# Kernel tuning notes

Measured on AMD Instinct MI355X. Metric: run time of the kernel, lower is better.

## Reference

```python
import jax, jax.numpy as jnp
import numpy as np

B, N, D, H, P = 4, 512, 256, 8, 3
HD = D // H
EPS = 1e-5

def _ln(x, g, b):
    m = jnp.mean(x, axis=-1, keepdims=True)
    v = jnp.var(x, axis=-1, keepdims=True)
    return (x - m) * jax.lax.rsqrt(v + EPS) * g + b

def setup_inputs() -> dict:
    key = jax.random.key(0)
    ks = jax.random.split(key, 12)
    s = lambda *sh: 1.0 / np.sqrt(sh[0])
    return {
        "x": jax.random.normal(ks[0], (B, N, D), jnp.float32),
        "mask": jax.random.randint(ks[1], (B, N), 0, 2).astype(bool),
        "pair_feat": jax.random.normal(ks[2], (B, N, N, P), jnp.float32),
        "Wqkv": jax.random.normal(ks[3], (D, 3 * D), jnp.float32) * s(D),
        "Wout": jax.random.normal(ks[4], (D, D), jnp.float32) * s(D),
        "bout": jnp.zeros((D,), jnp.float32),
        "Wp1": jax.random.normal(ks[5], (P, D), jnp.float32) * s(P),
        "bp1": jnp.zeros((D,), jnp.float32),
        "Wp2": jax.random.normal(ks[6], (D, H), jnp.float32) * s(D),
        "bp2": jnp.zeros((H,), jnp.float32),
        "Wf1": jax.random.normal(ks[7], (D, 4 * D), jnp.float32) * s(D),
        "bf1": jnp.zeros((4 * D,), jnp.float32),
        "Wf2": jax.random.normal(ks[8], (4 * D, D), jnp.float32) * s(4 * D),
        "bf2": jnp.zeros((D,), jnp.float32),
        "g1": jnp.ones((D,), jnp.float32), "b1": jnp.zeros((D,), jnp.float32),
        "g2": jnp.ones((D,), jnp.float32), "b2": jnp.zeros((D,), jnp.float32),
    }

def reference(x, mask, pair_feat, Wqkv, Wout, bout, Wp1, bp1, Wp2, bp2,
              Wf1, bf1, Wf2, bf2, g1, b1, g2, b2):
    b_, n_, d_ = x.shape
    scale = HD ** -0.5
    qkv = x @ Wqkv                                  # [B,N,3D]
    q, k, v = jnp.split(qkv, 3, axis=-1)
    q = q.reshape(b_, n_, H, HD)
    k = k.reshape(b_, n_, H, HD)
    v = v.reshape(b_, n_, H, HD)
    logits = jnp.einsum('bihd,bjhd->bhij', q, k) * scale
    # pairwise bias MLP -> per-head bias [B,H,N,N]
    bias = jax.nn.relu(pair_feat @ Wp1 + bp1) @ Wp2 + bp2   # [B,N,N,H]
    logits = logits + jnp.transpose(bias, (0, 3, 1, 2))
    key_mask = ~mask[:, None, None, :]               # [B,1,1,N]
    logits = jnp.where(key_mask, -1e9, logits)
    attn = jax.nn.softmax(logits, axis=-1)
    out = jnp.einsum('bhij,bjhd->bihd', attn, v).reshape(b_, n_, d_)
    out = out @ Wout + bout
    x = _ln(x + out, g1, b1)
    h = jax.nn.gelu(x @ Wf1 + bf1, approximate=False) @ Wf2 + bf2
    return _ln(x + h, g2, b2)
```

## Files before the change

### kernel.cpp

```cpp
#include <hip/hip_runtime.h>
#include <hip/hip_fp16.h>
#include <math.h>

typedef unsigned short u16;
typedef short s16x8 __attribute__((ext_vector_type(8)));
typedef _Float16 f16x8 __attribute__((ext_vector_type(8)));
typedef float f32x4 __attribute__((ext_vector_type(4)));
typedef unsigned int u32x2 __attribute__((ext_vector_type(2)));

constexpr int CB = 4, CN = 512, CD = 256, CH = 8, CHD = 32;
constexpr float CEPS = 1e-5f;
constexpr int M_ROWS = CB * CN;
constexpr float QSCALE = 0.17677669529663687f;

constexpr size_t O_XB    = 0;
constexpr size_t O_QB    = 1048576;
constexpr size_t O_KB    = 2097152;
constexpr size_t O_VT    = 3145728;
constexpr size_t O_WQKVT = 4194304;
constexpr size_t O_WOUTT = O_WQKVT + 393216;
constexpr size_t O_WF1T  = O_WOUTT + 131072;
constexpr size_t O_WF2T  = O_WF1T + 524288;
constexpr size_t O_WP2T  = O_WF2T + 524288;
constexpr size_t O_PACKED= O_WP2T + 8192;
constexpr size_t O_MASKD = O_PACKED + 4096;
constexpr size_t O_BIAS  = O_MASKD + 8192;
constexpr size_t O_AOUT  = O_BIAS + 16777216;
constexpr size_t O_H1B   = O_AOUT + 1048576;
constexpr size_t O_PRE1  = O_H1B + 4194304;
constexpr size_t O_PRE2  = O_PRE1 + 2097152;

__device__ inline u16 f2b(float f) {
  union { float f; unsigned u; } v{f};
  return (u16)((v.u + 0x7FFFu + ((v.u >> 16) & 1u)) >> 16);
}
__device__ inline float b2f(u16 b) {
  union { unsigned u; float f; } v{(unsigned)b << 16};
  return v.f;
}
__device__ inline f32x4 MFMA(s16x8 a, s16x8 b, f32x4 c) {
  return __builtin_amdgcn_mfma_f32_16x16x32_bf16(a, b, c, 0, 0, 0);
}
__device__ inline f32x4 MFMAH(f16x8 a, f16x8 b, f32x4 c) {
  return __builtin_amdgcn_mfma_f32_16x16x32_f16(a, b, c, 0, 0, 0);
}
__device__ inline unsigned cvtpk(float lo, float hi) {
  unsigned r;
  asm("v_cvt_pk_bf16_f32 %0, %1, %2" : "=v"(r) : "v"(lo), "v"(hi));
  return r;
}
__device__ inline unsigned pkmax0(unsigned a) {
  unsigned d;
  asm("v_pk_max_f16 %0, %1, 0" : "=v"(d) : "v"(a));
  return d;
}

__global__ __launch_bounds__(256) void prep_kernel(
    const float* __restrict__ x, const float* __restrict__ Wqkv,
    const float* __restrict__ Wout, const float* __restrict__ Wf1,
    const float* __restrict__ Wf2, const float* __restrict__ Wp2,
    const float* __restrict__ Wp1, const float* __restrict__ bp1,
    const unsigned char* __restrict__ maskraw,
    u16* __restrict__ xb, u16* __restrict__ wqkvt, u16* __restrict__ woutt,
    u16* __restrict__ wf1t, u16* __restrict__ wf2t, u16* __restrict__ wp2t,
    unsigned* __restrict__ packed, int* __restrict__ maskd) {
  __shared__ int mode_max;
  int blk = blockIdx.x, tid = threadIdx.x;
  if (blk < 256) {
    for (int t = tid; t < 512; t += 256) {
      float4 v = ((const float4*)x)[blk * 512 + t];
      u16 o0 = f2b(v.x), o1 = f2b(v.y), o2 = f2b(v.z), o3 = f2b(v.w);
      u32x2 w; w.x = (unsigned)o0 | ((unsigned)o1 << 16);
      w.y = (unsigned)o2 | ((unsigned)o3 << 16);
      *(u32x2*)(xb + (size_t)(blk * 512 + t) * 4) = w;
    }
  } else if (blk < 352) {
    int o0 = (blk - 256) * 2048;
    for (int t = tid; t < 2048; t += 256) {
      int o = o0 + t, n = o >> 8, k = o & 255;
      wqkvt[o] = f2b(Wqkv[k * 768 + n]);
    }
  } else if (blk < 384) {
    int o0 = (blk - 352) * 2048;
    for (int t = tid; t < 2048; t += 256) {
      int o = o0 + t, n = o >> 8, k = o & 255;
      woutt[o] = f2b(Wout[k * 256 + n]);
    }
  } else if (blk < 512) {
    int o0 = (blk - 384) * 2048;
    for (int t = tid; t < 2048; t += 256) {
      int o = o0 + t, n = o >> 8, k = o & 255;
      wf1t[o] = f2b(Wf1[k * 1024 + n]);
    }
  } else if (blk < 640) {
    int o0 = (blk - 512) * 2048;
    for (int t = tid; t < 2048; t += 256) {
      int o = o0 + t, n = o >> 10, k = o & 1023;
      wf2t[o] = f2b(Wf2[k * 256 + n]);
    }
  } else if (blk == 640) {
    for (int t = tid; t < 4096; t += 256) {
      int h = t >> 8, c = t & 255;
      wp2t[t] = (h < 8) ? __half_as_ushort(__float2half(Wp2[c * 8 + h])) : (u16)0;
    }
    if (tid < 128) {
      int p = tid * 2;
      unsigned w0 = (unsigned)__half_as_ushort(__float2half(Wp1[p]))
                  | ((unsigned)__half_as_ushort(__float2half(Wp1[p + 1])) << 16);
      unsigned w1 = (unsigned)__half_as_ushort(__float2half(Wp1[256 + p]))
                  | ((unsigned)__half_as_ushort(__float2half(Wp1[256 + p + 1])) << 16);
      unsigned w2 = (unsigned)__half_as_ushort(__float2half(Wp1[512 + p]))
                  | ((unsigned)__half_as_ushort(__float2half(Wp1[512 + p + 1])) << 16);
      unsigned bb = (unsigned)__half_as_ushort(__float2half(bp1[p]))
                  | ((unsigned)__half_as_ushort(__float2half(bp1[p + 1])) << 16);
      uint4 o; o.x = w0; o.y = w1; o.z = w2; o.w = bb;
      ((uint4*)packed)[tid] = o;
    }
  } else {
    if (tid == 0) mode_max = 0;
    __syncthreads();
    int lm = 0;
    for (int i = tid; i < CB*CN; i += 256)
      if ((i & 3) != 0) lm = max(lm, (int)maskraw[i]);
    atomicMax(&mode_max, lm);
    __syncthreads();
    int mv = mode_max;
    for (int i = tid; i < CB*CN; i += 256) {
      int val;
      if (mv == 0)      val = (((const int*)maskraw)[i] != 0);
      else if (mv == 1) val = (maskraw[i] != 0);
      else              val = (((const unsigned int*)maskraw)[i] != 0);
      maskd[i] = val;
    }
  }
}

__global__ __launch_bounds__(256) void qkv_pbias_kernel(
    const u16* __restrict__ A, const u16* __restrict__ Wt,
    u16* __restrict__ qb, u16* __restrict__ kb, u16* __restrict__ vt,
    const float* __restrict__ pf, const unsigned* __restrict__ packed,
    const u16* __restrict__ wp2t, const float* __restrict__ bp2,
    u16* __restrict__ biasout) {
  __shared__ uint4 smem[1024];
  const int blk = blockIdx.x, tid = threadIdx.x;
  const int lane = tid & 63, w = tid >> 6;
  if (blk < 384) {
    u16* As = (u16*)smem;
    u16* Bs = (u16*)smem + 64 * 64;
    const int wm = w >> 1, wn = w & 1;
    const int bm = (blk / 12) * 64, bn = (blk % 12) * 64;
    f32x4 fz = {0.f, 0.f, 0.f, 0.f};
    f32x4 acc[2][2] = {{fz, fz}, {fz, fz}};
    for (int k0 = 0; k0 < 256; k0 += 64) {
#pragma unroll
      for (int t = tid; t < 512; t += 256) {
        int r = t >> 3, s = t & 7;
        s16x8 v = *(const s16x8*)(A + (size_t)(bm + r) * 256 + k0 + s * 8);
        *(s16x8*)(As + r * 64 + ((s ^ (r & 7)) << 3)) = v;
      }
#pragma unroll
      for (int t = tid; t < 512; t += 256) {
        int r = t >> 3, s = t & 7;
        s16x8 v = *(const s16x8*)(Wt + (size_t)(bn + r) * 256 + k0 + s * 8);
        *(s16x8*)(Bs + r * 64 + ((s ^ (r & 7)) << 3)) = v;
      }
      __syncthreads();
#pragma unroll
      for (int ks = 0; ks < 2; ++ks) {
        s16x8 af[2], bf[2];
#pragma unroll
        for (int mf = 0; mf < 2; ++mf) {
          int r = wm * 32 + mf * 16 + (lane & 15);
          int s = ks * 4 + (lane >> 4);
          af[mf] = *(const s16x8*)(As + r * 64 + ((s ^ (r & 7)) << 3));
        }
#pragma unroll
        for (int nf = 0; nf < 2; ++nf) {
          int r = wn * 32 + nf * 16 + (lane & 15);
          int s = ks * 4 + (lane >> 4);
          bf[nf] = *(const s16x8*)(Bs + r * 64 + ((s ^ (r & 7)) << 3));
        }
#pragma unroll
        for (int mf = 0; mf < 2; ++mf)
#pragma unroll
          for (int nf = 0; nf < 2; ++nf)
            acc[mf][nf] = MFMA(af[mf], bf[nf], acc[mf][nf]);
      }
      __syncthreads();
    }
#pragma unroll
    for (int mf = 0; mf < 2; ++mf) {
#pragma unroll
      for (int nf = 0; nf < 2; ++nf) {
#pragma unroll
        for (int r = 0; r < 4; ++r) {
          int m = bm + wm * 32 + mf * 16 + (lane >> 4) * 4 + r;
          int n = bn + wn * 32 + nf * 16 + (lane & 15);
          float v = acc[mf][nf][r];
          if (n < 256) {
            qb[(size_t)m * 256 + n] = f2b(v * QSCALE);
          } else if (n < 512) {
            kb[(size_t)m * 256 + (n - 256)] = f2b(v);
          } else {
            int nv = n - 512, h = nv >> 5, d = nv & 31;
            int bb = m >> 9, j = m & 511;
            vt[(size_t)((bb * 8 + h) * 32 + d) * 512 + j] = f2b(v);
          }
        }
      }
    }
  } else {
    uint4* pk = smem;
    const int bid = blk - 384;
    const int b = bid >> 9, i = bid & 511;
    const int q = lane >> 4, hr = lane & 15;
    if (tid < 128) pk[tid] = ((const uint4*)packed)[tid];
    const float* pfb = pf + (size_t)(b * 512 + i) * 1536;
    __half2 f0d[8], f1d[8], f2d[8];
#pragma unroll
    for (int t = 0; t < 8; ++t) {
      int j = w * 128 + t * 16 + hr;
      f0d[t] = __float2half2_rn(pfb[j * 3 + 0]);
      f1d[t] = __float2half2_rn(pfb[j * 3 + 1]);
      f2d[t] = __float2half2_rn(pfb[j * 3 + 2]);
    }
    __syncthreads();
    f32x4 fz = {0.f, 0.f, 0.f, 0.f};
    f32x4 acc[8] = {fz, fz, fz, fz, fz, fz, fz, fz};
    for (int chunk = 0; chunk < 8; ++chunk) {
      f16x8 wfrag = *(const f16x8*)(wp2t + hr * 256 + chunk * 32 + q * 8);
      int pbase = chunk * 16 + q * 4;
      __half2 w0[4], w1[4], w2[4], bb[4];
#pragma unroll
      for (int p = 0; p < 4; ++p) {
        uint4 c = pk[pbase + p];
        w0[p] = *(const __half2*)&c.x;
        w1[p] = *(const __half2*)&c.y;
        w2[p] = *(const __half2*)&c.z;
        bb[p] = *(const __half2*)&c.w;
      }
#pragma unroll
      for (int t = 0; t < 8; ++t) {
        union { unsigned u[4]; f16x8 v; } af;
#pragma unroll
        for (int p = 0; p < 4; ++p) {
          __half2 h = __hfma2(f0d[t], w0[p], bb[p]);
          h = __hfma2(f1d[t], w1[p], h);
          h = __hfma2(f2d[t], w2[p], h);
          af.u[p] = pkmax0(*(const unsigned*)&h);
        }
        acc[t] = MFMAH(af.v, wfrag, acc[t]);
      }
    }
    if (hr < 8) {
      float bb = bp2[hr];
      size_t base = ((size_t)(b * 8 + hr) * 512 + i) * 512;
#pragma unroll
      for (int t = 0; t < 8; ++t) {
        int j0 = w * 128 + t * 16 + q * 4;
        u32x2 o;
        o.x = cvtpk(acc[t][0] + bb, acc[t][1] + bb);
        o.y = cvtpk(acc[t][2] + bb, acc[t][3] + bb);
        *(u32x2*)(biasout + base + j0) = o;
      }
    }
  }
}

__global__ __launch_bounds__(256) void mgemm_res(
    const u16* __restrict__ A, const u16* __restrict__ Wt,
    const float* __restrict__ bias, const float* __restrict__ R,
    float* __restrict__ outf, int N, int K) {
  __shared__ u16 As[32 * 64];
  __shared__ u16 Bs[64 * 64];
  const int tid = threadIdx.x;
  const int lane = tid & 63, w = tid >> 6;
  const int wm = w >> 1, wn = w & 1;
  const int bm = blockIdx.y * 32, bn = blockIdx.x * 64;
  f32x4 fz = {0.f, 0.f, 0.f, 0.f};
  f32x4 acc[2] = {fz, fz};
  for (int k0 = 0; k0 < K; k0 += 64) {
    for (int t = tid; t < 256; t += 256) {
      int r = t >> 3, s = t & 7;
      s16x8 v = *(const s16x8*)(A + (size_t)(bm + r) * K + k0 + s * 8);
      *(s16x8*)(As + r * 64 + ((s ^ (r & 7)) << 3)) = v;
    }
#pragma unroll
    for (int t = tid; t < 512; t += 256) {
      int r = t >> 3, s = t & 7;
      s16x8 v = *(const s16x8*)(Wt + (size_t)(bn + r) * K + k0 + s * 8);
      *(s16x8*)(Bs + r * 64 + ((s ^ (r & 7)) << 3)) = v;
    }
    __syncthreads();
#pragma unroll
    for (int ks = 0; ks < 2; ++ks) {
      int r = wm * 16 + (lane & 15);
      int s = ks * 4 + (lane >> 4);
      s16x8 af = *(const s16x8*)(As + r * 64 + ((s ^ (r & 7)) << 3));
#pragma unroll
      for (int nf = 0; nf < 2; ++nf) {
        int br = wn * 32 + nf * 16 + (lane & 15);
        s16x8 bf = *(const s16x8*)(Bs + br * 64 + ((s ^ (br & 7)) << 3));
        acc[nf] = MFMA(af, bf, acc[nf]);
      }
    }
    __syncthreads();
  }
#pragma unroll
  for (int nf = 0; nf < 2; ++nf) {
#pragma unroll
    for (int r = 0; r < 4; ++r) {
      int m = bm + wm * 16 + (lane >> 4) * 4 + r;
      int n = bn + wn * 32 + nf * 16 + (lane & 15);
      outf[(size_t)m * N + n] = acc[nf][r] + bias[n] + R[(size_t)m * N + n];
    }
  }
}

__global__ __launch_bounds__(256) void ffn1_kernel(
    const float* __restrict__ pre1, const u16* __restrict__ Wt,
    const float* __restrict__ bias, const float* __restrict__ g1,
    const float* __restrict__ b1, u16* __restrict__ outb) {
  __shared__ u16 As[64 * 64];
  __shared__ u16 Bs[64 * 64];
  __shared__ float rowm[64], rowr[64];
  const int tid = threadIdx.x;
  const int lane = tid & 63, w = tid >> 6;
  const int wm = w >> 1, wn = w & 1;
  const int bm = blockIdx.y * 64, bn = blockIdx.x * 64;
  {
    int r = tid >> 2, qd = tid & 3;
    const float4* pr = (const float4*)(pre1 + (size_t)(bm + r) * 256 + qd * 64);
    float s = 0.f, ss = 0.f;
#pragma unroll
    for (int u = 0; u < 16; ++u) {
      float4 v = pr[u];
      s += v.x + v.y + v.z + v.w;
      ss += v.x*v.x + v.y*v.y + v.z*v.z + v.w*v.w;
    }
    s += __shfl_xor(s, 1); ss += __shfl_xor(ss, 1);
    s += __shfl_xor(s, 2); ss += __shfl_xor(ss, 2);
    if (qd == 0) {
      float mean = s * (1.0f / 256.0f);
      float var  = ss * (1.0f / 256.0f) - mean * mean;
      rowm[r] = mean; rowr[r] = rsqrtf(var + CEPS);
    }
  }
  __syncthreads();
  f32x4 fz = {0.f, 0.f, 0.f, 0.f};
  f32x4 acc[2][2] = {{fz, fz}, {fz, fz}};
  for (int k0 = 0; k0 < 256; k0 += 64) {
#pragma unroll
    for (int t = tid; t < 512; t += 256) {
      int r = t >> 3, s = t & 7;
      float mean = rowm[r], rstd = rowr[r];
      const float4* pr = (const float4*)(pre1 + (size_t)(bm + r) * 256 + k0 + s * 8);
      float4 a0 = pr[0], a1 = pr[1];
      const float4* gp = (const float4*)(g1 + k0 + s * 8);
      const float4* bp = (const float4*)(b1 + k0 + s * 8);
      float4 g0 = gp[0], g1v = gp[1], c0 = bp[0], c1 = bp[1];
      union { unsigned u[4]; s16x8 v; } pk2;
      pk2.u[0] = cvtpk((a0.x-mean)*rstd*g0.x + c0.x, (a0.y-mean)*rstd*g0.y + c0.y);
      pk2.u[1] = cvtpk((a0.z-mean)*rstd*g0.z + c0.z, (a0.w-mean)*rstd*g0.w + c0.w);
      pk2.u[2] = cvtpk((a1.x-mean)*rstd*g1v.x + c1.x, (a1.y-mean)*rstd*g1v.y + c1.y);
      pk2.u[3] = cvtpk((a1.z-mean)*rstd*g1v.z + c1.z, (a1.w-mean)*rstd*g1v.w + c1.w);
      *(s16x8*)(As + r * 64 + ((s ^ (r & 7)) << 3)) = pk2.v;
    }
#pragma unroll
    for (int t = tid; t < 512; t += 256) {
      int r = t >> 3, s = t & 7;
      s16x8 v = *(const s16x8*)(Wt + (size_t)(bn + r) * 256 + k0 + s * 8);
      *(s16x8*)(Bs + r * 64 + ((s ^ (r & 7)) << 3)) = v;
    }
    __syncthreads();
#pragma unroll
    for (int ks = 0; ks < 2; ++ks) {
      s16x8 af[2], bf[2];
#pragma unroll
      for (int mf = 0; mf < 2; ++mf) {
        int r = wm * 32 + mf * 16 + (lane & 15);
        int s = ks * 4 + (lane >> 4);
        af[mf] = *(const s16x8*)(As + r * 64 + ((s ^ (r & 7)) << 3));
      }
#pragma unroll
      for (int nf = 0; nf < 2; ++nf) {
        int r = wn * 32 + nf * 16 + (lane & 15);
        int s = ks * 4 + (lane >> 4);
        bf[nf] = *(const s16x8*)(Bs + r * 64 + ((s ^ (r & 7)) << 3));
      }
#pragma unroll
      for (int mf = 0; mf < 2; ++mf)
#pragma unroll
        for (int nf = 0; nf < 2; ++nf)
          acc[mf][nf] = MFMA(af[mf], bf[nf], acc[mf][nf]);
    }
    __syncthreads();
  }
#pragma unroll
  for (int mf = 0; mf < 2; ++mf) {
#pragma unroll
    for (int nf = 0; nf < 2; ++nf) {
#pragma unroll
      for (int r = 0; r < 4; ++r) {
        int m = bm + wm * 32 + mf * 16 + (lane >> 4) * 4 + r;
        int n = bn + wn * 32 + nf * 16 + (lane & 15);
        float gv = acc[mf][nf][r] + bias[n];
        gv = 0.5f * gv * (1.0f + erff(gv * 0.70710678118654752f));
        outb[(size_t)m * 1024 + n] = f2b(gv);
      }
    }
  }
}

__global__ __launch_bounds__(256) void ffn2_kernel(
    const u16* __restrict__ A, const u16* __restrict__ Wt,
    const float* __restrict__ bias, const float* __restrict__ pre1,
    const float* __restrict__ g1, const float* __restrict__ b1,
    float* __restrict__ outf) {
  __shared__ u16 As[32 * 64];
  __shared__ u16 Bs[64 * 64];
  __shared__ float rowm[32], rowr[32];
  const int tid = threadIdx.x;
  const int lane = tid & 63, w = tid >> 6;
  const int wm = w >> 1, wn = w & 1;
  const int bm = blockIdx.y * 32, bn = blockIdx.x * 64;
  {
    int r = tid >> 3, od = tid & 7;
    const float4* pr = (const float4*)(pre1 + (size_t)(bm + r) * 256 + od * 32);
    float s = 0.f, ss = 0.f;
#pragma unroll
    for (int u = 0; u < 8; ++u) {
      float4 v = pr[u];
      s += v.x + v.y + v.z + v.w;
      ss += v.x*v.x + v.y*v.y + v.z*v.z + v.w*v.w;
    }
    s += __shfl_xor(s, 1); ss += __shfl_xor(ss, 1);
    s += __shfl_xor(s, 2); ss += __shfl_xor(ss, 2);
    s += __shfl_xor(s, 4); ss += __shfl_xor(ss, 4);
    if (od == 0) {
      float mean = s * (1.0f / 256.0f);
      float var  = ss * (1.0f / 256.0f) - mean * mean;
      rowm[r] = mean; rowr[r] = rsqrtf(var + CEPS);
    }
  }
  __syncthreads();
  f32x4 fz = {0.f, 0.f, 0.f, 0.f};
  f32x4 acc[2] = {fz, fz};
  for (int k0 = 0; k0 < 1024; k0 += 64) {
    for (int t = tid; t < 256; t += 256) {
      int r = t >> 3, s = t & 7;
      s16x8 v = *(const s16x8*)(A + (size_t)(bm + r) * 1024 + k0 + s * 8);
      *(s16x8*)(As + r * 64 + ((s ^ (r & 7)) << 3)) = v;
    }
#pragma unroll
    for (int t = tid; t < 512; t += 256) {
      int r = t >> 3, s = t & 7;
      s16x8 v = *(const s16x8*)(Wt + (size_t)(bn + r) * 1024 + k0 + s * 8);
      *(s16x8*)(Bs + r * 64 + ((s ^ (r & 7)) << 3)) = v;
    }
    __syncthreads();
#pragma unroll
    for (int ks = 0; ks < 2; ++ks) {
      int r = wm * 16 + (lane & 15);
      int s = ks * 4 + (lane >> 4);
      s16x8 af = *(const s16x8*)(As + r * 64 + ((s ^ (r & 7)) << 3));
#pragma unroll
      for (int nf = 0; nf < 2; ++nf) {
        int br = wn * 32 + nf * 16 + (lane & 15);
        s16x8 bf = *(const s16x8*)(Bs + br * 64 + ((s ^ (br & 7)) << 3));
        acc[nf] = MFMA(af, bf, acc[nf]);
      }
    }
    __syncthreads();
  }
#pragma unroll
  for (int nf = 0; nf < 2; ++nf) {
#pragma unroll
    for (int r = 0; r < 4; ++r) {
      int m = bm + wm * 16 + (lane >> 4) * 4 + r;
      int n = bn + wn * 32 + nf * 16 + (lane & 15);
      float mean = rowm[m - bm], rstd = rowr[m - bm];
      float xr = (pre1[(size_t)m * 256 + n] - mean) * rstd * g1[n] + b1[n];
      outf[(size_t)m * 256 + n] = acc[nf][r] + bias[n] + xr;
    }
  }
}

__global__ __launch_bounds__(512) void flash_kernel(
    const u16* __restrict__ qb, const u16* __restrict__ kb,
    const u16* __restrict__ vt, const u16* __restrict__ biasin,
    const int* __restrict__ maskd, u16* __restrict__ aout) {
  const int i0 = blockIdx.x * 64, h = blockIdx.y, b = blockIdx.z;
  const int tid = threadIdx.x;
  const int lane = tid & 63, w = tid >> 6;
  const int mf = w & 3, jhalf = w >> 2;
  __shared__ u16 qs[64 * 32];
  __shared__ u16 ksh[128 * 32];
  __shared__ u16 vs[32 * 128];
  __shared__ u16 bs[64 * 128];
  __shared__ u16 ps[8][16 * 64];
  __shared__ float cmb[4][2][16][2];
  for (int t = tid; t < 256; t += 512) {
    int r = t >> 2, s = t & 3;
    s16x8 v = *(const s16x8*)(qb + (size_t)(b * 512 + i0 + r) * 256 + h * 32 + s * 8);
    *(s16x8*)(qs + r * 32 + ((s ^ (r & 3)) << 3)) = v;
  }
  f32x4 fz = {0.f, 0.f, 0.f, 0.f};
  f32x4 oacc[2] = {fz, fz};
  float mrun[4] = {-3e38f, -3e38f, -3e38f, -3e38f};
  float lrun[4] = {0.f, 0.f, 0.f, 0.f};
  const int* mrow = maskd + b * 512;
  const int jj0 = jhalf * 64;
  for (int jc = 0; jc < 4; ++jc) {
    int j0 = jc * 128;
    for (int t = tid; t < 512; t += 512) {
      int r = t >> 2, s = t & 3;
      s16x8 v = *(const s16x8*)(kb + (size_t)(b * 512 + j0 + r) * 256 + h * 32 + s * 8);
      *(s16x8*)(ksh + r * 32 + ((s ^ (r & 3)) << 3)) = v;
    }
    for (int t = tid; t < 512; t += 512) {
      int r = t >> 4, s = t & 15;
      s16x8 v = *(const s16x8*)(vt + (size_t)((b * 8 + h) * 32 + r) * 512 + j0 + s * 8);
      *(s16x8*)(vs + r * 128 + (((s & 8) | ((s & 7) ^ (r & 7))) << 3)) = v;
    }
#pragma unroll
    for (int t = tid; t < 1024; t += 512) {
      int r = t >> 4, s = t & 15;
      s16x8 v = *(const s16x8*)(biasin + ((size_t)((b * 8 + h) * 512 + i0 + r)) * 512 + j0 + s * 8);
      *(s16x8*)(bs + r * 128 + (((s & 8) | ((s & 7) ^ (r & 7))) << 3)) = v;
    }
    __syncthreads();
    int mk[4];
#pragma unroll
    for (int jf = 0; jf < 4; ++jf)
      mk[jf] = mrow[j0 + jj0 + jf * 16 + (lane & 15)];
    int arow = mf * 16 + (lane & 15);
    s16x8 af = *(const s16x8*)(qs + arow * 32 + (((lane >> 4) ^ (arow & 3)) << 3));
    f32x4 sm[4];
#pragma unroll
    for (int jf = 0; jf < 4; ++jf) {
      int brow = jj0 + jf * 16 + (lane & 15);
      s16x8 bfr = *(const s16x8*)(ksh + brow * 32 + (((lane >> 4) ^ (brow & 3)) << 3));
      sm[jf] = MFMA(af, bfr, fz);
    }
    int il = mf * 16 + (lane >> 4) * 4;
#pragma unroll
    for (int jf = 0; jf < 4; ++jf) {
#pragma unroll
      for (int r = 0; r < 4; ++r) {
        int i_loc = il + r;
        int jb = jj0 + jf * 16 + (lane & 15);
        int slot = jb >> 3;
        float bv = b2f(bs[i_loc * 128 + (((slot & 8) | ((slot & 7) ^ (i_loc & 7))) << 3) + (jb & 7)]);
        float sval = sm[jf][r] + bv;
        sm[jf][r] = mk[jf] ? sval : -1e9f;
      }
    }
    float mx[4];
#pragma unroll
    for (int r = 0; r < 4; ++r)
      mx[r] = fmaxf(fmaxf(sm[0][r], sm[1][r]), fmaxf(sm[2][r], sm[3][r]));
#pragma unroll
    for (int d = 1; d < 16; d <<= 1)
#pragma unroll
      for (int r = 0; r < 4; ++r) mx[r] = fmaxf(mx[r], __shfl_xor(mx[r], d));
    float psl[4] = {0.f, 0.f, 0.f, 0.f};
#pragma unroll
    for (int jf = 0; jf < 4; ++jf)
#pragma unroll
      for (int r = 0; r < 4; ++r) {
        float p = __expf(sm[jf][r] - mx[r]);
        sm[jf][r] = p; psl[r] += p;
      }
#pragma unroll
    for (int d = 1; d < 16; d <<= 1)
#pragma unroll
      for (int r = 0; r < 4; ++r) psl[r] += __shfl_xor(psl[r], d);
    if ((lane & 15) == 0) {
#pragma unroll
      for (int r = 0; r < 4; ++r) {
        int row = (lane >> 4) * 4 + r;
        cmb[mf][jhalf][row][0] = mx[r];
        cmb[mf][jhalf][row][1] = psl[r];
      }
    }
    __syncthreads();
    float selfs[4];
#pragma unroll
    for (int r = 0; r < 4; ++r) {
      int row = (lane >> 4) * 4 + r;
      float omx = cmb[mf][1 - jhalf][row][0];
      float ops = cmb[mf][1 - jhalf][row][1];
      float tm = fmaxf(mx[r], omx);
      float nm = fmaxf(mrun[r], tm);
      float sc = __expf(mrun[r] - nm);
      selfs[r] = __expf(mx[r] - nm);
      float ptile = psl[r] * selfs[r] + ops * __expf(omx - nm);
      lrun[r] = lrun[r] * sc + ptile;
      mrun[r] = nm;
      oacc[0][r] *= sc; oacc[1][r] *= sc;
    }
    u16* pw = &ps[w][0];
#pragma unroll
    for (int jf = 0; jf < 4; ++jf) {
      int jcol = jf * 16 + (lane & 15);
      int slot = jcol >> 3, el = jcol & 7;
#pragma unroll
      for (int r = 0; r < 4; ++r) {
        int row = (lane >> 4) * 4 + r;
        pw[row * 64 + ((slot ^ (row & 7)) << 3) + el] = f2b(sm[jf][r] * selfs[r]);
      }
    }
#pragma unroll
    for (int kw = 0; kw < 2; ++kw) {
      int prow = lane & 15;
      s16x8 pa = *(const s16x8*)(pw + prow * 64 + (((kw * 4 + (lane >> 4)) ^ (prow & 7)) << 3));
#pragma unroll
      for (int df = 0; df < 2; ++df) {
        int drow = df * 16 + (lane & 15);
        int jcol = jj0 + kw * 32 + ((lane >> 4) << 3);
        int slot = jcol >> 3;
        s16x8 vb = *(const s16x8*)(vs + drow * 128 + (((slot & 8) | ((slot & 7) ^ (drow & 7))) << 3));
        oacc[df] = MFMA(pa, vb, oacc[df]);
      }
    }
    __syncthreads();
  }
  float* obuf = (float*)bs;
  if (jhalf == 1) {
#pragma unroll
    for (int r = 0; r < 4; ++r) {
      int row = mf * 16 + (lane >> 4) * 4 + r;
#pragma unroll
      for (int df = 0; df < 2; ++df)
        obuf[row * 33 + df * 16 + (lane & 15)] = oacc[df][r];
    }
  }
  __syncthreads();
  if (jhalf == 0) {
#pragma unroll
    for (int r = 0; r < 4; ++r) {
      float inv = 1.0f / lrun[r];
      int row = mf * 16 + (lane >> 4) * 4 + r;
      int i = i0 + row;
#pragma unroll
      for (int df = 0; df < 2; ++df) {
        int d = df * 16 + (lane & 15);
        float o = (oacc[df][r] + obuf[row * 33 + d]) * inv;
        aout[(size_t)(b * 512 + i) * 256 + h * 32 + d] = f2b(o);
      }
    }
  }
}

__global__ __launch_bounds__(256) void ln_kernel(
    const float* __restrict__ in, const float* __restrict__ g,
    const float* __restrict__ be, float* __restrict__ op) {
  int row = blockIdx.x * 4 + (threadIdx.x >> 6);
  int lane = threadIdx.x & 63;
  const float* x = in + (size_t)row * CD;
  float4 v = *(const float4*)&x[lane * 4];
  float s  = v.x + v.y + v.z + v.w;
  float ss = v.x*v.x + v.y*v.y + v.z*v.z + v.w*v.w;
#pragma unroll
  for (int off = 32; off > 0; off >>= 1) {
    s  += __shfl_xor(s, off);
    ss += __shfl_xor(ss, off);
  }
  float mean = s * (1.0f / CD);
  float var  = ss * (1.0f / CD) - mean * mean;
  float inv  = rsqrtf(var + CEPS);
  float4 gg = *(const float4*)&g[lane * 4];
  float4 bb = *(const float4*)&be[lane * 4];
  float4 o;
  o.x = (v.x - mean) * inv * gg.x + bb.x;
  o.y = (v.y - mean) * inv * gg.y + bb.y;
  o.z = (v.z - mean) * inv * gg.z + bb.z;
  o.w = (v.w - mean) * inv * gg.w + bb.w;
  *(float4*)&op[(size_t)row * CD + lane * 4] = o;
}

extern "C" void kernel_launch(void* const* d_in, const int* in_sizes, int n_in,
                              void* d_out, int out_size, void* d_ws, size_t ws_size,
                              hipStream_t stream) {
  (void)in_sizes; (void)n_in; (void)out_size; (void)ws_size;
  const float* x    = (const float*)d_in[0];
  const void*  mask = d_in[1];
  const float* pf   = (const float*)d_in[2];
  const float* Wqkv = (const float*)d_in[3];
  const float* Wout = (const float*)d_in[4];
  const float* bout = (const float*)d_in[5];
  const float* Wp1  = (const float*)d_in[6];
  const float* bp1  = (const float*)d_in[7];
  const float* Wp2  = (const float*)d_in[8];
  const float* bp2  = (const float*)d_in[9];
  const float* Wf1  = (const float*)d_in[10];
  const float* bf1  = (const float*)d_in[11];
  const float* Wf2  = (const float*)d_in[12];
  const float* bf2  = (const float*)d_in[13];
  const float* g1   = (const float*)d_in[14];
  const float* b1   = (const float*)d_in[15];
  const float* g2   = (const float*)d_in[16];
  const float* b2   = (const float*)d_in[17];

  char* ws = (char*)d_ws;
  u16* xb     = (u16*)(ws + O_XB);
  u16* qb     = (u16*)(ws + O_QB);
  u16* kb     = (u16*)(ws + O_KB);
  u16* vt     = (u16*)(ws + O_VT);
  u16* wqkvt  = (u16*)(ws + O_WQKVT);
  u16* woutt  = (u16*)(ws + O_WOUTT);
  u16* wf1t   = (u16*)(ws + O_WF1T);
  u16* wf2t   = (u16*)(ws + O_WF2T);
  u16* wp2t   = (u16*)(ws + O_WP2T);
  unsigned* packed = (unsigned*)(ws + O_PACKED);
  int* maskd  = (int*)(ws + O_MASKD);
  u16* biasb  = (u16*)(ws + O_BIAS);
  u16* aout   = (u16*)(ws + O_AOUT);
  u16* h1b    = (u16*)(ws + O_H1B);
  float* pre1 = (float*)(ws + O_PRE1);
  float* pre2 = (float*)(ws + O_PRE2);
  float* out  = (float*)d_out;

  hipLaunchKernelGGL(prep_kernel, dim3(642), dim3(256), 0, stream,
                     x, Wqkv, Wout, Wf1, Wf2, Wp2, Wp1, bp1,
                     (const unsigned char*)mask,
                     xb, wqkvt, woutt, wf1t, wf2t, wp2t, packed, maskd);
  hipLaunchKernelGGL(qkv_pbias_kernel, dim3(2432), dim3(256), 0, stream,
                     xb, wqkvt, qb, kb, vt,
                     pf, packed, wp2t, bp2, biasb);
  hipLaunchKernelGGL(flash_kernel, dim3(8, 8, 4), dim3(512), 0, stream,
                     qb, kb, vt, biasb, maskd, aout);
  hipLaunchKernelGGL(mgemm_res, dim3(4, 64), dim3(256), 0, stream,
                     aout, woutt, bout, x, pre1, 256, 256);
  hipLaunchKernelGGL(ffn1_kernel, dim3(16, 32), dim3(256), 0, stream,
                     pre1, wf1t, bf1, g1, b1, h1b);
  hipLaunchKernelGGL(ffn2_kernel, dim3(4, 64), dim3(256), 0, stream,
                     h1b, wf2t, bf2, pre1, g1, b1, pre2);
  hipLaunchKernelGGL(ln_kernel, dim3(M_ROWS / 4), dim3(256), 0, stream,
                     pre2, g2, b2, out);
}
```

Measured before the change: 99.90 us.

## Load attention bias directly into registers and stage pair features through LDS

In the flash kernel, the per-head bias tile is now read from global memory straight into registers in MFMA accumulator layout instead of being staged through a 16KB shared buffer. This frees LDS, which may help occupancy, and removes a shared-memory round trip. The output combine buffer now reuses the P scratch area. The pair-bias block also copies its pair-feature row into shared memory with coalesced float4 loads before doing strided per-thread reads. The bias loads are now 2-byte scattered global reads, which coalesce less well.

```diff
diff --git a/kernel.cpp b/kernel.cpp
--- a/kernel.cpp
+++ b/kernel.cpp
@@ -211,20 +211,23 @@
     }
   } else {
     uint4* pk = smem;
+    float* pfl = (float*)(smem + 128);
     const int bid = blk - 384;
     const int b = bid >> 9, i = bid & 511;
     const int q = lane >> 4, hr = lane & 15;
     if (tid < 128) pk[tid] = ((const uint4*)packed)[tid];
-    const float* pfb = pf + (size_t)(b * 512 + i) * 1536;
+    const float4* pfr = (const float4*)(pf + (size_t)(b * 512 + i) * 1536);
+#pragma unroll
+    for (int t = tid; t < 384; t += 256) ((float4*)pfl)[t] = pfr[t];
+    __syncthreads();
     __half2 f0d[8], f1d[8], f2d[8];
 #pragma unroll
     for (int t = 0; t < 8; ++t) {
       int j = w * 128 + t * 16 + hr;
-      f0d[t] = __float2half2_rn(pfb[j * 3 + 0]);
-      f1d[t] = __float2half2_rn(pfb[j * 3 + 1]);
-      f2d[t] = __float2half2_rn(pfb[j * 3 + 2]);
-    }
-    __syncthreads();
+      f0d[t] = __float2half2_rn(pfl[j * 3 + 0]);
+      f1d[t] = __float2half2_rn(pfl[j * 3 + 1]);
+      f2d[t] = __float2half2_rn(pfl[j * 3 + 2]);
+    }
     f32x4 fz = {0.f, 0.f, 0.f, 0.f};
     f32x4 acc[8] = {fz, fz, fz, fz, fz, fz, fz, fz};
     for (int chunk = 0; chunk < 8; ++chunk) {
@@ -497,7 +500,6 @@
   __shared__ u16 qs[64 * 32];
   __shared__ u16 ksh[128 * 32];
   __shared__ u16 vs[32 * 128];
-  __shared__ u16 bs[64 * 128];
   __shared__ u16 ps[8][16 * 64];
   __shared__ float cmb[4][2][16][2];
   for (int t = tid; t < 256; t += 512) {
@@ -511,6 +513,9 @@
   float lrun[4] = {0.f, 0.f, 0.f, 0.f};
   const int* mrow = maskd + b * 512;
   const int jj0 = jhalf * 64;
+  const int il = mf * 16 + (lane >> 4) * 4;
+  const u16* bbase = biasin + ((size_t)((b * 8 + h) * 512 + i0 + il)) * 512
+                   + jj0 + (lane & 15);
   for (int jc = 0; jc < 4; ++jc) {
     int j0 = jc * 128;
     for (int t = tid; t < 512; t += 512) {
@@ -523,12 +528,12 @@
       s16x8 v = *(const s16x8*)(vt + (size_t)((b * 8 + h) * 32 + r) * 512 + j0 + s * 8);
       *(s16x8*)(vs + r * 128 + (((s & 8) | ((s & 7) ^ (r & 7))) << 3)) = v;
     }
-#pragma unroll
-    for (int t = tid; t < 1024; t += 512) {
-      int r = t >> 4, s = t & 15;
-      s16x8 v = *(const s16x8*)(biasin + ((size_t)((b * 8 + h) * 512 + i0 + r)) * 512 + j0 + s * 8);
-      *(s16x8*)(bs + r * 128 + (((s & 8) | ((s & 7) ^ (r & 7))) << 3)) = v;
-    }
+    u16 bvr[4][4];
+#pragma unroll
+    for (int jf = 0; jf < 4; ++jf)
+#pragma unroll
+      for (int r = 0; r < 4; ++r)
+        bvr[jf][r] = bbase[(size_t)r * 512 + j0 + jf * 16];
     __syncthreads();
     int mk[4];
 #pragma unroll
@@ -543,16 +548,11 @@
       s16x8 bfr = *(const s16x8*)(ksh + brow * 32 + (((lane >> 4) ^ (brow & 3)) << 3));
       sm[jf] = MFMA(af, bfr, fz);
     }
-    int il = mf * 16 + (lane >> 4) * 4;
 #pragma unroll
     for (int jf = 0; jf < 4; ++jf) {
 #pragma unroll
       for (int r = 0; r < 4; ++r) {
-        int i_loc = il + r;
-        int jb = jj0 + jf * 16 + (lane & 15);
-        int slot = jb >> 3;
-        float bv = b2f(bs[i_loc * 128 + (((slot & 8) | ((slot & 7) ^ (i_loc & 7))) << 3) + (jb & 7)]);
-        float sval = sm[jf][r] + bv;
+        float sval = sm[jf][r] + b2f(bvr[jf][r]);
         sm[jf][r] = mk[jf] ? sval : -1e9f;
       }
     }
@@ -626,7 +626,7 @@
     }
     __syncthreads();
   }
-  float* obuf = (float*)bs;
+  float* obuf = (float*)&ps[0][0];
   if (jhalf == 1) {
 #pragma unroll
     for (int r = 0; r < 4; ++r) {
```

Result: no change. 99.99 us (+0.1%).
